# Kernel optimization log

Hardware: AMD Instinct MI355X
Metric: run time of the kernel (lower is better)

The kernel has to match this reference:

```python
import jax, jax.numpy as jnp
import numpy as np

HIDDEN = 1024
HEADS = 16
HEAD_DIM = HIDDEN // HEADS
SCALE = HEAD_DIM ** (-0.5)


def setup_inputs() -> dict:
    key = jax.random.key(0)
    ks = jax.random.split(key, 5)
    B, N, C = 8, 1024, HIDDEN
    x = jax.random.normal(ks[0], (B, N, C), dtype=jnp.float32)
    # torch nn.Linear params: weight [out, in], bias [out]
    w_in = jax.random.normal(ks[1], (3 * C, C), dtype=jnp.float32) * (C ** -0.5)
    b_in = jax.random.normal(ks[2], (3 * C,), dtype=jnp.float32) * 0.02
    w_out = jax.random.normal(ks[3], (C, C), dtype=jnp.float32) * (C ** -0.5)
    b_out = jax.random.normal(ks[4], (C,), dtype=jnp.float32) * 0.02
    return {"x": x, "w_in": w_in, "b_in": b_in, "w_out": w_out, "b_out": b_out}


def reference(x, w_in, b_in, w_out, b_out):
    B, N, C = x.shape
    H, D = HEADS, HEAD_DIM
    # in_proj: [B,N,3C] -> (3,B,H,N,D)
    qkv = x @ w_in.T + b_in
    qkv = qkv.reshape(B, N, 3, H, D).transpose(2, 0, 3, 1, 4)
    q, k, v = qkv[0], qkv[1], qkv[2]
    # attention scores scaled after QK^T (same math as scaling q)
    attn = jnp.einsum("bhnd,bhmd->bhnm", q, k) * SCALE
    attn = jax.nn.softmax(attn, axis=-1)
    out = jnp.einsum("bhnm,bhmd->bhnd", attn, v)  # [B,H,N,D]
    out = out.transpose(0, 2, 1, 3).reshape(B, N, C)
    return out @ w_out.T + b_out
```

## Files before the change

kernel.cpp:

```cpp
#include <hip/hip_runtime.h>


typedef __attribute__((ext_vector_type(8))) __bf16 bf16x8;
typedef __attribute__((ext_vector_type(4))) __bf16 bf16x4;
typedef __attribute__((ext_vector_type(4))) float f32x4;
typedef __attribute__((ext_vector_type(4))) short short4v;

__device__ __forceinline__ f32x4 mfma16(bf16x8 a, bf16x8 b, f32x4 c) {
  return __builtin_amdgcn_mfma_f32_16x16x32_bf16(a, b, c, 0, 0, 0);
}

#if __has_builtin(__builtin_amdgcn_mfma_f32_16x16x16bf16_1k)
__device__ __forceinline__ f32x4 mfma_pv(bf16x4 a, bf16x4 b, f32x4 c) {
  short4v as = __builtin_bit_cast(short4v, a);
  short4v bs = __builtin_bit_cast(short4v, b);
  return __builtin_amdgcn_mfma_f32_16x16x16bf16_1k(as, bs, c, 0, 0, 0);
}
#else
__device__ __forceinline__ f32x4 mfma_pv(bf16x4 a, bf16x4 b, f32x4 c) {
  __bf16 z = (__bf16)0.f;
  bf16x8 a8 = {a[0], a[1], a[2], a[3], z, z, z, z};
  bf16x8 b8 = {b[0], b[1], b[2], b[3], z, z, z, z};
  return mfma16(a8, b8, c);
}
#endif

__device__ __forceinline__ float fexp2(float x) {
#if __has_builtin(__builtin_amdgcn_exp2f)
  return __builtin_amdgcn_exp2f(x);
#else
  return exp2f(x);
#endif
}

typedef __attribute__((address_space(1))) const unsigned int gu32;
typedef __attribute__((address_space(3))) unsigned int lu32;

__device__ __forceinline__ void async16(const void* g, void* l) {
  __builtin_amdgcn_global_load_lds((gu32*)g, (lu32*)l, 16, 0, 0);
}

__global__ __launch_bounds__(256) void cvt_all(const float* __restrict__ x,
                                               __bf16* __restrict__ xb,
                                               const float* __restrict__ wi,
                                               __bf16* __restrict__ wib,
                                               const float* __restrict__ wo,
                                               __bf16* __restrict__ wob) {
  int blk = blockIdx.x;
  const float* in;
  __bf16* out;
  int base;
  if (blk < 4096)      { in = x;  out = xb;  base = 0; }
  else if (blk < 5632) { in = wi; out = wib; base = 4096; }
  else                 { in = wo; out = wob; base = 5632; }
  int i = ((blk - base) * 256 + threadIdx.x) * 8;
  float4 a = *(const float4*)(in + i);
  float4 b = *(const float4*)(in + i + 4);
  bf16x8 o;
  o[0] = (__bf16)a.x; o[1] = (__bf16)a.y; o[2] = (__bf16)a.z; o[3] = (__bf16)a.w;
  o[4] = (__bf16)b.x; o[5] = (__bf16)b.y; o[6] = (__bf16)b.z; o[7] = (__bf16)b.w;
  *(bf16x8*)(out + i) = o;
}

template <bool WRITE_VT>
__global__ __launch_bounds__(512, 4) void gemm1(const __bf16* __restrict__ A,
                                                const __bf16* __restrict__ Bm,
                                                const float* __restrict__ bias,
                                                __bf16* __restrict__ C,
                                                __bf16* __restrict__ vt) {
  __shared__ char lds[49152];
  const int t = threadIdx.x;
  const int wv = t >> 6, lane = t & 63;
  const int q16 = lane & 15, quad = lane >> 4;
  const int wm = wv >> 1, wn = wv & 1;
  const int bid = blockIdx.x;
  const long m0 = (long)(bid & 31) * 256;
  const long n0 = (long)(bid >> 5) * 128;

  const int sr4 = t >> 2;
  const int gc = (t & 3) ^ ((sr4 >> 1) & 3);
  const int ldst = wv * 1024;

  const __bf16* srcA0 = A + (m0 + sr4) * 1024 + gc * 8;
  const __bf16* srcA1 = A + (m0 + 128 + sr4) * 1024 + gc * 8;
  const __bf16* srcB  = Bm + (n0 + sr4) * 1024 + gc * 8;

  const int raB = (wm * 64 + q16) * 64 + ((quad ^ ((q16 >> 1) & 3)) * 16);
  const int rbB = (wn * 64 + q16) * 64 + ((quad ^ ((q16 >> 1) & 3)) * 16);

  f32x4 zero = {0.f, 0.f, 0.f, 0.f};
  f32x4 acc[4][4];
#pragma unroll
  for (int i = 0; i < 4; ++i)
#pragma unroll
    for (int j = 0; j < 4; ++j) acc[i][j] = zero;

  async16(srcA0, lds + ldst);
  async16(srcA1, lds + 8192 + ldst);
  async16(srcB, lds + 16384 + ldst);
  __syncthreads();

  int cur = 0;
#pragma unroll 1
  for (int t32 = 0; t32 < 32; ++t32) {
    char* Ac = lds + cur * 24576;
    char* Bc = Ac + 16384;

    if (t32 < 31) {
      char* S = lds + (cur ^ 1) * 24576;
      const int kt = (t32 + 1) * 32;
      async16(srcA0 + kt, S + ldst);
      async16(srcA1 + kt, S + 8192 + ldst);
      async16(srcB + kt, S + 16384 + ldst);
    }

    bf16x8 af[4], bfr[4];
#pragma unroll
    for (int mi = 0; mi < 4; ++mi)
      af[mi] = *(const bf16x8*)(Ac + raB + mi * 1024);
#pragma unroll
    for (int nj = 0; nj < 4; ++nj)
      bfr[nj] = *(const bf16x8*)(Bc + rbB + nj * 1024);

    __builtin_amdgcn_s_setprio(1);
#pragma unroll
    for (int mi = 0; mi < 4; ++mi)
#pragma unroll
      for (int nj = 0; nj < 4; ++nj)
        acc[mi][nj] = mfma16(af[mi], bfr[nj], acc[mi][nj]);
    __builtin_amdgcn_s_setprio(0);

    __syncthreads();
    cur ^= 1;
  }

  if (WRITE_VT && n0 >= 2048) {
    const int b = (int)(m0 >> 10);
    const int nbase = (int)(m0 & 1023) + wm * 64;
#pragma unroll
    for (int nj = 0; nj < 4; ++nj) {
      int col = (int)n0 + wn * 64 + nj * 16 + q16;
      int cc = col - 2048;
      int h = cc >> 6, d = cc & 63;
      float bs = bias[col];
      __bf16* vrow = vt + (((long)(b * 16 + h)) << 16) + (long)d * 1024;
#pragma unroll
      for (int mi = 0; mi < 4; ++mi) {
        int n = nbase + mi * 16 + quad * 4;
        bf16x4 o;
#pragma unroll
        for (int r = 0; r < 4; ++r) o[r] = (__bf16)(acc[mi][nj][r] + bs);
        *(bf16x4*)(vrow + n) = o;
      }
    }
  } else {
#pragma unroll
    for (int nj = 0; nj < 4; ++nj) {
      long col = n0 + wn * 64 + nj * 16 + q16;
      float bs = bias[col];
#pragma unroll
      for (int mi = 0; mi < 4; ++mi) {
        long rowb = m0 + wm * 64 + mi * 16 + quad * 4;
#pragma unroll
        for (int r = 0; r < 4; ++r) {
          float v = acc[mi][nj][r] + bs;
          C[(rowb + r) * 3072 + col] = (__bf16)v;
        }
      }
    }
  }
}

__global__ __launch_bounds__(256, 4) void gemm2(const __bf16* __restrict__ A,
                                                const __bf16* __restrict__ Bm,
                                                const float* __restrict__ bias,
                                                float* __restrict__ C) {
  __shared__ char lds[24576];
  const int t = threadIdx.x;
  const int wv = t >> 6, lane = t & 63;
  const int q16 = lane & 15, quad = lane >> 4;
  const int wm = wv >> 1, wn = wv & 1;
  const long m0 = (long)blockIdx.x * 64;
  const long n0 = (long)blockIdx.y * 128;

  const int sr2 = t >> 2;
  const int gc = (t & 3) ^ ((sr2 >> 1) & 3);
  const int ldst = wv * 1024;

  const __bf16* srcA  = A + (m0 + sr2) * 1024 + gc * 8;
  const __bf16* srcB0 = Bm + (n0 + sr2) * 1024 + gc * 8;
  const __bf16* srcB1 = Bm + (n0 + 64 + sr2) * 1024 + gc * 8;

  const int raB = (wm * 32 + q16) * 64 + ((quad ^ ((q16 >> 1) & 3)) * 16);
  const int rbB = (wn * 64 + q16) * 64 + ((quad ^ ((q16 >> 1) & 3)) * 16);

  f32x4 zero = {0.f, 0.f, 0.f, 0.f};
  f32x4 acc[2][4];
#pragma unroll
  for (int i = 0; i < 2; ++i)
#pragma unroll
    for (int j = 0; j < 4; ++j) acc[i][j] = zero;

  async16(srcA, lds + ldst);
  async16(srcB0, lds + 4096 + ldst);
  async16(srcB1, lds + 8192 + ldst);
  __syncthreads();

  int cur = 0;
#pragma unroll 1
  for (int t32 = 0; t32 < 32; ++t32) {
    char* Ac = lds + cur * 12288;
    char* Bc = Ac + 4096;

    if (t32 < 31) {
      char* S = lds + (cur ^ 1) * 12288;
      const int kt = (t32 + 1) * 32;
      async16(srcA + kt, S + ldst);
      async16(srcB0 + kt, S + 4096 + ldst);
      async16(srcB1 + kt, S + 8192 + ldst);
    }

    bf16x8 af[2], bfr[4];
#pragma unroll
    for (int mi = 0; mi < 2; ++mi)
      af[mi] = *(const bf16x8*)(Ac + raB + mi * 1024);
#pragma unroll
    for (int nj = 0; nj < 4; ++nj)
      bfr[nj] = *(const bf16x8*)(Bc + rbB + nj * 1024);

    __builtin_amdgcn_s_setprio(1);
#pragma unroll
    for (int mi = 0; mi < 2; ++mi)
#pragma unroll
      for (int nj = 0; nj < 4; ++nj)
        acc[mi][nj] = mfma16(af[mi], bfr[nj], acc[mi][nj]);
    __builtin_amdgcn_s_setprio(0);

    __syncthreads();
    cur ^= 1;
  }

#pragma unroll
  for (int nj = 0; nj < 4; ++nj) {
    long col = n0 + wn * 64 + nj * 16 + q16;
    float bs = bias[col];
#pragma unroll
    for (int mi = 0; mi < 2; ++mi) {
      long rowb = m0 + wm * 32 + mi * 16 + quad * 4;
#pragma unroll
      for (int r = 0; r < 4; ++r) {
        float v = acc[mi][nj][r] + bs;
        C[(rowb + r) * 1024 + col] = v;
      }
    }
  }
}

__global__ __launch_bounds__(256) void attn_kernel(const __bf16* __restrict__ qkv,
                                                   const __bf16* __restrict__ vt,
                                                   __bf16* __restrict__ ao) {
  __shared__ char lds[16384];
  const int t = threadIdx.x;
  const int wv = t >> 6, lane = t & 63;
  const int q16 = lane & 15, quad = lane >> 4;
  const int bh = blockIdx.x;
  const int b = bh >> 4, h = bh & 15;
  const int q0 = blockIdx.y * 64;
  const long rowbase = (long)b * 1024;

  bf16x8 qf0, qf1;
  {
    long qrow = rowbase + q0 + wv * 16 + q16;
    const __bf16* qp = qkv + qrow * 3072 + h * 64 + quad * 8;
    qf0 = *(const bf16x8*)qp;
    qf1 = *(const bf16x8*)(qp + 32);
#pragma unroll
    for (int j = 0; j < 8; ++j) {
      qf0[j] = (__bf16)((float)qf0[j] * 0.18033688f);
      qf1[j] = (__bf16)((float)qf1[j] * 0.18033688f);
    }
  }

  f32x4 zero = {0.f, 0.f, 0.f, 0.f};
  f32x4 oacc[4];
#pragma unroll
  for (int dt = 0; dt < 4; ++dt) oacc[dt] = zero;
  float lcol = 0.f;

  const int sr8 = t >> 3;
  const int sgc8 = (t & 7) ^ (sr8 & 7);
  const int sr2 = t >> 2;
  const int gc4 = (t & 3) ^ ((sr2 >> 1) & 3);
  const int ldst = wv * 1024;

  const __bf16* kbase = qkv + (rowbase + sr8) * 3072 + 1024 + h * 64 + sgc8 * 8;
  const __bf16* vbase = vt + (long)bh * 65536 + (long)sr2 * 1024 + gc4 * 8;

  const int sw = q16 & 7;
  const int vg = (q16 >> 1) & 3;

  async16(kbase, lds + ldst);
  async16(vbase, lds + 8192 + ldst);
  __syncthreads();

  int cur = 0;
#pragma unroll 1
  for (int it = 0; it < 32; ++it) {
    char* KsB = lds + cur * 4096;
    char* VtB = lds + 8192 + cur * 4096;

    if (it < 31) {
      const int kv = (it + 1) * 32;
      async16(kbase + (long)kv * 3072, lds + (cur ^ 1) * 4096 + ldst);
      async16(vbase + kv, lds + 8192 + (cur ^ 1) * 4096 + ldst);
    }

    f32x4 sacc[2];
#pragma unroll
    for (int nt = 0; nt < 2; ++nt) sacc[nt] = zero;
#pragma unroll
    for (int nt = 0; nt < 2; ++nt) {
      int kvr = nt * 16 + q16;
      bf16x8 kf0 = *(const bf16x8*)(KsB + kvr * 128 + ((quad ^ sw) * 16));
      bf16x8 kf1 = *(const bf16x8*)(KsB + kvr * 128 + (((4 + quad) ^ sw) * 16));
      sacc[nt] = mfma16(kf0, qf0, sacc[nt]);
      sacc[nt] = mfma16(kf1, qf1, sacc[nt]);
    }

    bf16x4 pf[2];
#pragma unroll
    for (int nt = 0; nt < 2; ++nt)
#pragma unroll
      for (int r = 0; r < 4; ++r) {
        float p = fexp2(sacc[nt][r]);
        lcol += p;
        pf[nt][r] = (__bf16)p;
      }

#pragma unroll
    for (int nt = 0; nt < 2; ++nt) {
      int c = (((nt * 2 + (quad >> 1)) ^ vg) * 16) + (quad & 1) * 8;
#pragma unroll
      for (int dt = 0; dt < 4; ++dt) {
        bf16x4 vf = *(const bf16x4*)(VtB + (dt * 16 + q16) * 64 + c);
        oacc[dt] = mfma_pv(pf[nt], vf, oacc[dt]);
      }
    }

    __syncthreads();
    cur ^= 1;
  }

  lcol += __shfl_xor(lcol, 16);
  lcol += __shfl_xor(lcol, 32);
  float inv = 1.0f / lcol;
#pragma unroll
  for (int r = 0; r < 4; ++r) {
    float ir = __shfl(inv, quad * 4 + r);
    long orow = rowbase + q0 + wv * 16 + quad * 4 + r;
#pragma unroll
    for (int dt = 0; dt < 4; ++dt)
      ao[orow * 1024 + h * 64 + dt * 16 + q16] = (__bf16)(oacc[dt][r] * ir);
  }
}

extern "C" void kernel_launch(void* const* d_in, const int* in_sizes, int n_in,
                              void* d_out, int out_size, void* d_ws, size_t ws_size,
                              hipStream_t stream) {
  const float* x     = (const float*)d_in[0];
  const float* w_in  = (const float*)d_in[1];
  const float* b_in  = (const float*)d_in[2];
  const float* w_out = (const float*)d_in[3];
  const float* b_out = (const float*)d_in[4];
  float* out = (float*)d_out;

  char* ws = (char*)d_ws;
  __bf16* xb   = (__bf16*)(ws);
  __bf16* wib  = (__bf16*)(ws + 16777216);
  __bf16* wob  = (__bf16*)(ws + 23068672);
  __bf16* qkvb = (__bf16*)(ws + 25165824);
  __bf16* aob  = (__bf16*)(ws + 75497472);
  __bf16* vtg  = (__bf16*)d_out;

  cvt_all<<<6144, 256, 0, stream>>>(x, xb, w_in, wib, w_out, wob);
  gemm1<true><<<768, 512, 0, stream>>>(xb, wib, b_in, qkvb, vtg);
  attn_kernel<<<dim3(128, 16), 256, 0, stream>>>(qkvb, vtg, aob);
  gemm2<<<dim3(128, 8), 256, 0, stream>>>(aob, wob, b_out, out);
}
```

Baseline: 242.3 us.

## Process two query tiles per attention block with 64-row KV tiles

Each attention block now handles 128 query rows (two 64-row halves per wave set) and loads 64-row K/V tiles. This halves the grid and reuses each K/V tile for twice as many queries, cutting global K/V traffic. It also drops the double-buffered async prefetch in favour of a single buffer with two barriers per tile, so load latency is no longer overlapped with compute. The V tile layout and swizzle change to match the wider tile.

Measured after the change: 229.7 us. 5.2% less time.

```diff
diff --git a/kernel.cpp b/kernel.cpp
--- a/kernel.cpp
+++ b/kernel.cpp
@@ -256,111 +256,111 @@
   }
 }
 
-__global__ __launch_bounds__(256) void attn_kernel(const __bf16* __restrict__ qkv,
-                                                   const __bf16* __restrict__ vt,
-                                                   __bf16* __restrict__ ao) {
-  __shared__ char lds[16384];
+__global__ __launch_bounds__(256, 4) void attn_kernel(const __bf16* __restrict__ qkv,
+                                                      const __bf16* __restrict__ vt,
+                                                      __bf16* __restrict__ ao) {
+  __shared__ __bf16 Ks[64 * 64];
+  __shared__ __bf16 Vt[64 * 64];
   const int t = threadIdx.x;
   const int wv = t >> 6, lane = t & 63;
   const int q16 = lane & 15, quad = lane >> 4;
   const int bh = blockIdx.x;
   const int b = bh >> 4, h = bh & 15;
-  const int q0 = blockIdx.y * 64;
+  const int q0 = blockIdx.y * 128;
   const long rowbase = (long)b * 1024;
 
-  bf16x8 qf0, qf1;
-  {
-    long qrow = rowbase + q0 + wv * 16 + q16;
+  bf16x8 qf0[2], qf1[2];
+#pragma unroll
+  for (int qh = 0; qh < 2; ++qh) {
+    long qrow = rowbase + q0 + qh * 64 + wv * 16 + q16;
     const __bf16* qp = qkv + qrow * 3072 + h * 64 + quad * 8;
-    qf0 = *(const bf16x8*)qp;
-    qf1 = *(const bf16x8*)(qp + 32);
+    bf16x8 a = *(const bf16x8*)qp;
+    bf16x8 c = *(const bf16x8*)(qp + 32);
 #pragma unroll
     for (int j = 0; j < 8; ++j) {
-      qf0[j] = (__bf16)((float)qf0[j] * 0.18033688f);
-      qf1[j] = (__bf16)((float)qf1[j] * 0.18033688f);
-    }
+      a[j] = (__bf16)((float)a[j] * 0.18033688f);
+      c[j] = (__bf16)((float)c[j] * 0.18033688f);
+    }
+    qf0[qh] = a;
+    qf1[qh] = c;
   }
 
   f32x4 zero = {0.f, 0.f, 0.f, 0.f};
-  f32x4 oacc[4];
-#pragma unroll
-  for (int dt = 0; dt < 4; ++dt) oacc[dt] = zero;
-  float lcol = 0.f;
-
-  const int sr8 = t >> 3;
-  const int sgc8 = (t & 7) ^ (sr8 & 7);
-  const int sr2 = t >> 2;
-  const int gc4 = (t & 3) ^ ((sr2 >> 1) & 3);
-  const int ldst = wv * 1024;
-
-  const __bf16* kbase = qkv + (rowbase + sr8) * 3072 + 1024 + h * 64 + sgc8 * 8;
-  const __bf16* vbase = vt + (long)bh * 65536 + (long)sr2 * 1024 + gc4 * 8;
-
+  f32x4 oacc[2][4];
+#pragma unroll
+  for (int qh = 0; qh < 2; ++qh)
+#pragma unroll
+    for (int dt = 0; dt < 4; ++dt) oacc[qh][dt] = zero;
+  float lcol0 = 0.f, lcol1 = 0.f;
+
+  char* KsB = (char*)Ks;
+  char* VtB = (char*)Vt;
+  const int sr = t >> 3;
+  const int sgc = (t & 7) ^ (sr & 7);
   const int sw = q16 & 7;
-  const int vg = (q16 >> 1) & 3;
-
-  async16(kbase, lds + ldst);
-  async16(vbase, lds + 8192 + ldst);
-  __syncthreads();
-
-  int cur = 0;
-#pragma unroll 1
-  for (int it = 0; it < 32; ++it) {
-    char* KsB = lds + cur * 4096;
-    char* VtB = lds + 8192 + cur * 4096;
-
-    if (it < 31) {
-      const int kv = (it + 1) * 32;
-      async16(kbase + (long)kv * 3072, lds + (cur ^ 1) * 4096 + ldst);
-      async16(vbase + kv, lds + 8192 + (cur ^ 1) * 4096 + ldst);
-    }
-
-    f32x4 sacc[2];
-#pragma unroll
-    for (int nt = 0; nt < 2; ++nt) sacc[nt] = zero;
-#pragma unroll
-    for (int nt = 0; nt < 2; ++nt) {
-      int kvr = nt * 16 + q16;
-      bf16x8 kf0 = *(const bf16x8*)(KsB + kvr * 128 + ((quad ^ sw) * 16));
-      bf16x8 kf1 = *(const bf16x8*)(KsB + kvr * 128 + (((4 + quad) ^ sw) * 16));
-      sacc[nt] = mfma16(kf0, qf0, sacc[nt]);
-      sacc[nt] = mfma16(kf1, qf1, sacc[nt]);
-    }
-
-    bf16x4 pf[2];
-#pragma unroll
-    for (int nt = 0; nt < 2; ++nt)
-#pragma unroll
-      for (int r = 0; r < 4; ++r) {
-        float p = fexp2(sacc[nt][r]);
-        lcol += p;
-        pf[nt][r] = (__bf16)p;
-      }
-
-#pragma unroll
-    for (int nt = 0; nt < 2; ++nt) {
-      int c = (((nt * 2 + (quad >> 1)) ^ vg) * 16) + (quad & 1) * 8;
-#pragma unroll
-      for (int dt = 0; dt < 4; ++dt) {
-        bf16x4 vf = *(const bf16x4*)(VtB + (dt * 16 + q16) * 64 + c);
-        oacc[dt] = mfma_pv(pf[nt], vf, oacc[dt]);
-      }
-    }
-
+
+  for (int kv0 = 0; kv0 < 1024; kv0 += 64) {
     __syncthreads();
-    cur ^= 1;
-  }
-
-  lcol += __shfl_xor(lcol, 16);
-  lcol += __shfl_xor(lcol, 32);
-  float inv = 1.0f / lcol;
-#pragma unroll
-  for (int r = 0; r < 4; ++r) {
-    float ir = __shfl(inv, quad * 4 + r);
-    long orow = rowbase + q0 + wv * 16 + quad * 4 + r;
-#pragma unroll
-    for (int dt = 0; dt < 4; ++dt)
-      ao[orow * 1024 + h * 64 + dt * 16 + q16] = (__bf16)(oacc[dt][r] * ir);
+    const __bf16* kg = qkv + (rowbase + kv0 + sr) * 3072 + 1024 + h * 64 + sgc * 8;
+    async16(kg, KsB + wv * 1024);
+    async16(kg + (long)32 * 3072, KsB + 4096 + wv * 1024);
+    const __bf16* vg = vt + (long)bh * 65536 + (long)sr * 1024 + kv0 + sgc * 8;
+    async16(vg, VtB + wv * 1024);
+    async16(vg + (long)32 * 1024, VtB + 4096 + wv * 1024);
+    __syncthreads();
+
+#pragma unroll
+    for (int qh = 0; qh < 2; ++qh) {
+      f32x4 sacc[4];
+#pragma unroll
+      for (int nt = 0; nt < 4; ++nt) sacc[nt] = zero;
+#pragma unroll
+      for (int nt = 0; nt < 4; ++nt) {
+        int kvr = nt * 16 + q16;
+        bf16x8 kf0 = *(const bf16x8*)(KsB + kvr * 128 + ((quad ^ sw) * 16));
+        bf16x8 kf1 = *(const bf16x8*)(KsB + kvr * 128 + (((4 + quad) ^ sw) * 16));
+        sacc[nt] = mfma16(kf0, qf0[qh], sacc[nt]);
+        sacc[nt] = mfma16(kf1, qf1[qh], sacc[nt]);
+      }
+
+      bf16x4 pf[4];
+      float lc = 0.f;
+#pragma unroll
+      for (int nt = 0; nt < 4; ++nt)
+#pragma unroll
+        for (int r = 0; r < 4; ++r) {
+          float p = fexp2(sacc[nt][r]);
+          lc += p;
+          pf[nt][r] = (__bf16)p;
+        }
+      if (qh == 0) lcol0 += lc; else lcol1 += lc;
+
+#pragma unroll
+      for (int nt = 0; nt < 4; ++nt) {
+        int c = ((nt * 2 + (quad >> 1)) ^ sw) * 16 + (quad & 1) * 8;
+#pragma unroll
+        for (int dt = 0; dt < 4; ++dt) {
+          bf16x4 vf = *(const bf16x4*)(VtB + (dt * 16 + q16) * 128 + c);
+          oacc[qh][dt] = mfma_pv(pf[nt], vf, oacc[qh][dt]);
+        }
+      }
+    }
+  }
+
+#pragma unroll
+  for (int qh = 0; qh < 2; ++qh) {
+    float lcol = qh == 0 ? lcol0 : lcol1;
+    lcol += __shfl_xor(lcol, 16);
+    lcol += __shfl_xor(lcol, 32);
+    float inv = 1.0f / lcol;
+#pragma unroll
+    for (int r = 0; r < 4; ++r) {
+      float ir = __shfl(inv, quad * 4 + r);
+      long orow = rowbase + q0 + qh * 64 + wv * 16 + quad * 4 + r;
+#pragma unroll
+      for (int dt = 0; dt < 4; ++dt)
+        ao[orow * 1024 + h * 64 + dt * 16 + q16] = (__bf16)(oacc[qh][dt][r] * ir);
+    }
   }
 }
 
@@ -384,6 +384,6 @@
 
   cvt_all<<<6144, 256, 0, stream>>>(x, xb, w_in, wib, w_out, wob);
   gemm1<true><<<768, 512, 0, stream>>>(xb, wib, b_in, qkvb, vtg);
-  attn_kernel<<<dim3(128, 16), 256, 0, stream>>>(qkvb, vtg, aob);
+  attn_kernel<<<dim3(128, 8), 256, 0, stream>>>(qkvb, vtg, aob);
   gemm2<<<dim3(128, 8), 256, 0, stream>>>(aob, wob, b_out, out);
 }
```
